# Kernel optimization log

Measured on AMD Instinct MI355X. Metric: run time of the kernel, lower is better.

Reference implementation:

```python
import jax, jax.numpy as jnp
import numpy as np

V = 25426          # tgt_vocab_size
D = 256            # d_model
H = 8              # heads
DH = 2048          # dim_head (d_ff passed positionally as d_head in source)
INNER = H * DH     # 16384
CLS = V            # cls token id (same value for t1 and t2 in source)
MASK_TOK = V + 2   # mask token id
VT = V + 3         # total embedding vocab


def _pos_encoding(n, d):
    pos = np.arange(n, dtype=np.float32)[:, None]
    div = np.exp(np.arange(0, d, 2, dtype=np.float32) * (-np.log(10000.0) / d))
    pe = np.zeros((n, d), dtype=np.float32)
    pe[:, 0::2] = np.sin(pos * div)
    pe[:, 1::2] = np.cos(pos * div)
    return jnp.asarray(pe)


def _layernorm(x, g, b, eps=1e-5):
    m = x.mean(-1, keepdims=True)
    v = ((x - m) ** 2).mean(-1, keepdims=True)
    return (x - m) / jnp.sqrt(v + eps) * g + b


def _cross_attn(x, ctx, pad_mask, Wq, Wk, Wv, Wo, bo):
    # x: [B,N,D], ctx: [B,M,Dc], pad_mask: [B,M] True = masked
    B, N, _ = x.shape
    M = ctx.shape[1]
    scale = DH ** -0.5
    q = (x @ Wq).reshape(B, N, H, DH)
    k = (ctx @ Wk).reshape(B, M, H, DH)
    v = (ctx @ Wv).reshape(B, M, H, DH)
    sim = jnp.einsum('bihd,bjhd->bhij', q, k) * scale  # [B,H,N,M]
    neg = -jnp.finfo(sim.dtype).max
    sim = jnp.where(pad_mask[:, None, None, :], neg, sim)
    attn = jax.nn.softmax(sim, axis=-1)
    out = jnp.einsum('bhij,bjhd->bihd', attn, v).reshape(B, N, INNER)
    return out @ Wo + bo


def _decoder(x, tgt_pad, src_mask, enc_output, p):
    a = _cross_attn(x, x, tgt_pad, p['Wq_s'], p['Wk_s'], p['Wv_s'], p['Wo_s'], p['bo_s'])
    x = _layernorm(x + a, p['g1'], p['be1'])
    a = _cross_attn(x, enc_output, src_mask, p['Wq_c'], p['Wk_c'], p['Wv_c'], p['Wo_c'], p['bo_c'])
    x = _layernorm(x + a, p['g2'], p['be2'])
    f = jax.nn.gelu(x @ p['W1'] + p['b1'], approximate=False) @ p['W2'] + p['b2']
    x = _layernorm(x + f, p['g3'], p['be3'])
    return x


def setup_inputs() -> dict:
    key = jax.random.key(0)
    ks = jax.random.split(key, 32)
    B, S, L = 2, 1024, 767
    d = {
        'src_input_id': jax.random.randint(ks[0], (B, S), 0, V),
        'tgt_input_id_t1': jax.random.randint(ks[1], (B, L), 0, V),
        'tgt_input_id_t2': jax.random.randint(ks[2], (B, L), 0, V),
        'original_lens': jax.random.randint(ks[3], (B,), 1, L),
        'enc_output': jax.random.normal(ks[4], (B, S, D), dtype=jnp.float32),
    }
    emb = jax.random.normal(ks[5], (VT, D), dtype=jnp.float32) * 0.02
    d['token_emb'] = emb.at[0].set(0.0)  # padding_idx=0
    s = 0.02
    d['Wq_s'] = jax.random.normal(ks[6], (D, INNER)) * s
    d['Wk_s'] = jax.random.normal(ks[7], (D, INNER)) * s
    d['Wv_s'] = jax.random.normal(ks[8], (D, INNER)) * s
    d['Wo_s'] = jax.random.normal(ks[9], (INNER, D)) * s
    d['bo_s'] = jnp.zeros((D,), jnp.float32)
    d['Wq_c'] = jax.random.normal(ks[10], (D, INNER)) * s
    d['Wk_c'] = jax.random.normal(ks[11], (D, INNER)) * s
    d['Wv_c'] = jax.random.normal(ks[12], (D, INNER)) * s
    d['Wo_c'] = jax.random.normal(ks[13], (INNER, D)) * s
    d['bo_c'] = jnp.zeros((D,), jnp.float32)
    d['W1'] = jax.random.normal(ks[14], (D, D)) * s  # Mlp hidden collapses to D (source bug)
    d['b1'] = jnp.zeros((D,), jnp.float32)
    d['W2'] = jax.random.normal(ks[15], (D, D)) * s
    d['b2'] = jnp.zeros((D,), jnp.float32)
    for i, n in enumerate(['g1', 'g2', 'g3']):
        d[n] = jnp.ones((D,), jnp.float32)
    for n in ['be1', 'be2', 'be3']:
        d[n] = jnp.zeros((D,), jnp.float32)
    d['Wfc'] = jax.random.normal(ks[16], (D, V)) * s
    d['bfc'] = jnp.zeros((V,), jnp.float32)
    return d


def reference(src_input_id, tgt_input_id_t1, tgt_input_id_t2, original_lens,
              enc_output, token_emb,
              Wq_s, Wk_s, Wv_s, Wo_s, bo_s,
              Wq_c, Wk_c, Wv_c, Wo_c, bo_c,
              W1, b1, W2, b2, g1, be1, g2, be2, g3, be3, Wfc, bfc):
    p = dict(Wq_s=Wq_s, Wk_s=Wk_s, Wv_s=Wv_s, Wo_s=Wo_s, bo_s=bo_s,
             Wq_c=Wq_c, Wk_c=Wk_c, Wv_c=Wv_c, Wo_c=Wo_c, bo_c=bo_c,
             W1=W1, b1=b1, W2=W2, b2=b2, g1=g1, be1=be1, g2=g2, be2=be2, g3=g3, be3=be3)
    B = tgt_input_id_t1.shape[0]
    cls = jnp.full((B, 1), CLS, dtype=tgt_input_id_t1.dtype)
    t1 = jnp.concatenate([cls, tgt_input_id_t1], axis=1)
    t2 = jnp.concatenate([cls, tgt_input_id_t2], axis=1)
    tgt = jnp.concatenate([t1, t2], axis=1)          # [B, T]
    tgt_pad = tgt == 0
    src_mask = src_input_id == 0
    # generate=True path: mask positions where id==mask_token or id==0
    tgt_mask = (tgt == MASK_TOK) | (tgt == 0)
    tgt_ids = jnp.where(tgt_mask, MASK_TOK, tgt)
    x = token_emb[tgt_ids]                            # [B, T, D]
    pe = _pos_encoding(x.shape[1], D)
    x = 2.0 * x + pe[None, :, :]                      # prepare_tokens: x + (x + pe), faithful to source
    x = _decoder(x, tgt_pad, src_mask, enc_output, p)
    logits = x @ Wfc + bfc
    return logits[:, 1:, :], x[:, 0, :]
```

## Files before the change

### kernel.cpp

```cpp
#include <hip/hip_runtime.h>
#include <hip/hip_bf16.h>
#include <float.h>
#include <math.h>

#define BB 2
#define SS 1024
#define LL 767
#define TT 1536
#define DD 256
#define HH 8
#define DHD 2048
#define INNER_ 16384
#define VV 25426
#define VPAD 25472
#define CLS_TOK 25426
#define MASK_TOKEN 25428
#define ROWS (BB*TT)
#define SROWS (BB*SS)

typedef __attribute__((ext_vector_type(8))) __bf16 bf16x8;
typedef __attribute__((ext_vector_type(4))) float f32x4;

__device__ __forceinline__ unsigned short f2bu(float f) {
    union { float f; unsigned u; } v; v.f = f;
    unsigned r = v.u + 0x7fff + ((v.u >> 16) & 1);
    return (unsigned short)(r >> 16);
}
__device__ __forceinline__ float bu2f(unsigned short u) {
    union { unsigned u; float f; } v; v.u = ((unsigned)u) << 16;
    return v.f;
}

__device__ __forceinline__ void gload16(const void* g, void* l) {
    __builtin_amdgcn_global_load_lds(
        (const __attribute__((address_space(1))) void*)g,
        (__attribute__((address_space(3))) void*)l, 16, 0, 0);
}


__global__ __launch_bounds__(256) void embed_kernel(
    const int* __restrict__ t1, const int* __restrict__ t2,
    const float* __restrict__ emb, float* __restrict__ x,
    unsigned short* __restrict__ xb, unsigned char* __restrict__ tgt_pad)
{
    int t = blockIdx.x, b = blockIdx.y, d = threadIdx.x;
    int raw;
    if (t == 0)            raw = CLS_TOK;
    else if (t <= LL)      raw = t1[b * LL + (t - 1)];
    else if (t == LL + 1)  raw = CLS_TOK;
    else                   raw = t2[b * LL + (t - LL - 2)];
    int id = (raw == 0 || raw == MASK_TOKEN) ? MASK_TOKEN : raw;
    int i = d >> 1;
    float ang = (float)t * expf(-0.03597789208f * (float)(2 * i));
    float pe = (d & 1) ? cosf(ang) : sinf(ang);
    float val = 2.f * emb[(long long)id * DD + d] + pe;
    long long idx = ((long long)(b * TT + t)) * DD + d;
    x[idx] = val;
    xb[idx] = f2bu(val);
    if (d == 0) tgt_pad[b * TT + t] = (raw == 0) ? 1 : 0;
}

__global__ __launch_bounds__(256) void masks_kernel(
    const int* __restrict__ src, unsigned char* __restrict__ m, int* __restrict__ rm)
{
    int i = blockIdx.x * 256 + threadIdx.x;
    if (i < SROWS) m[i] = (src[i] == 0) ? 1 : 0;
    if (i < ROWS) {
        int b = i / TT, t = i % TT;
        rm[i] = (t == 0) ? -1 : (b * (TT - 1) + t - 1);
    }
}

__global__ __launch_bounds__(256) void copycls_kernel(
    const float* __restrict__ x, float* __restrict__ out2)
{
    int b = blockIdx.x, d = threadIdx.x;
    out2[b * DD + d] = x[(long long)b * TT * DD + d];
}

__global__ __launch_bounds__(256) void conv_bf16v4(
    const float* __restrict__ in, unsigned short* __restrict__ out)
{
    size_t i = ((size_t)blockIdx.x * 256 + threadIdx.x) * 4;
    float4 v = *reinterpret_cast<const float4*>(in + i);
    ushort4 u;
    u.x = f2bu(v.x); u.y = f2bu(v.y); u.z = f2bu(v.z); u.w = f2bu(v.w);
    *reinterpret_cast<ushort4*>(out + i) = u;
}

__global__ __launch_bounds__(256) void convW6(
    const float* __restrict__ w0, const float* __restrict__ w1,
    const float* __restrict__ w2, const float* __restrict__ w3,
    const float* __restrict__ w4, const float* __restrict__ w5,
    unsigned short* __restrict__ dst)
{
    int seg = blockIdx.y;
    const float* s = seg == 0 ? w0 : seg == 1 ? w1 : seg == 2 ? w2 :
                     seg == 3 ? w3 : seg == 4 ? w4 : w5;
    size_t i = ((size_t)blockIdx.x * 256 + threadIdx.x) * 4;
    float4 v = *reinterpret_cast<const float4*>(s + i);
    ushort4 u;
    u.x = f2bu(v.x); u.y = f2bu(v.y); u.z = f2bu(v.z); u.w = f2bu(v.w);
    *reinterpret_cast<ushort4*>(dst + (size_t)seg * ((size_t)DD * INNER_) + i) = u;
}

__global__ __launch_bounds__(256) void transpose_conv(
    const float* __restrict__ in, unsigned short* __restrict__ out,
    int R, int Cin, int Nout)
{
    __shared__ float t[32][33];
    int k0 = blockIdx.x * 32, n0 = blockIdx.y * 32;
#pragma unroll
    for (int i = 0; i < 4; ++i) {
        int k = k0 + threadIdx.y + i * 8;
        int n = n0 + threadIdx.x;
        t[threadIdx.y + i * 8][threadIdx.x] = (n < Cin) ? in[(size_t)k * Cin + n] : 0.f;
    }
    __syncthreads();
#pragma unroll
    for (int i = 0; i < 4; ++i) {
        int n = n0 + threadIdx.y + i * 8;
        int k = k0 + threadIdx.x;
        out[(size_t)n * R + k] = f2bu(t[threadIdx.x][threadIdx.y + i * 8]);
    }
}

template<int STORE, int SPLITK>
__global__ __launch_bounds__(256) void gemm_bt(
    const unsigned short* __restrict__ A, int lda,
    const unsigned short* __restrict__ B, int ldb,
    void* __restrict__ Cv, int ldc,
    int M, int N, int K, float alpha, int zs,
    long long sAb, long long sAh, long long sBb, long long sBh,
    long long sCb, long long sCh,
    const float* __restrict__ bias, const int* __restrict__ rowmap)
{
    __shared__ unsigned short As[8192];
    __shared__ unsigned short Bs[8192];
    const int tid = threadIdx.x;
    const int w = tid >> 6, l = tid & 63;
    const int m0 = blockIdx.x * 128, n0 = blockIdx.y * 128;

    int kbeg = 0, kend = K;
    long long czoff = 0;
    if (SPLITK > 1) {
        constexpr int KSH = (SPLITK == 8) ? 3 : (SPLITK == 4) ? 2 : (SPLITK == 2) ? 1 : 0;
        int kidx = blockIdx.z & (SPLITK - 1);
        int zh = blockIdx.z >> KSH;
        int kc = K / SPLITK;
        kbeg = kidx * kc; kend = kbeg + kc;
        A += zh * sAh;
        B += zh * sBh;
        czoff = zh * sCh;
    } else {
        int zb = blockIdx.z >> zs;
        int zh = blockIdx.z - (zb << zs);
        A += zb * sAb + zh * sAh;
        B += zb * sBb + zh * sBh;
        czoff = zb * sCb + zh * sCh;
    }

    const int wr = (w >> 1) << 6, wc = (w & 1) << 6;
    const int lrow = l & 15, lk = l >> 4;

    const int sro = (w << 3) + (l >> 3);
    const int sko = (((l & 7) ^ (l >> 3)) << 3);
    const int ldst = (w << 10) + (l << 4);

    f32x4 acc[4][4];
#pragma unroll
    for (int mi = 0; mi < 4; ++mi)
#pragma unroll
        for (int ni = 0; ni < 4; ++ni)
            acc[mi][ni] = (f32x4){0.f, 0.f, 0.f, 0.f};

    for (int kt = kbeg; kt < kend; kt += 64) {
#pragma unroll
        for (int j = 0; j < 4; ++j)
            gload16(A + (size_t)(m0 + sro + j * 32) * lda + kt + sko,
                    (char*)As + (j << 12) + ldst);
#pragma unroll
        for (int j = 0; j < 4; ++j)
            gload16(B + (size_t)(n0 + sro + j * 32) * ldb + kt + sko,
                    (char*)Bs + (j << 12) + ldst);
        __syncthreads();

#pragma unroll
        for (int kk = 0; kk < 2; ++kk) {
            const int slot = (kk << 2) + lk;
            bf16x8 af[4], bfr[4];
#pragma unroll
            for (int mi = 0; mi < 4; ++mi) {
                int ra = wr + (mi << 4) + lrow;
                af[mi] = *reinterpret_cast<const bf16x8*>(
                    (const char*)As + (ra << 7) + ((slot ^ (ra & 7)) << 4));
            }
#pragma unroll
            for (int ni = 0; ni < 4; ++ni) {
                int rb = wc + (ni << 4) + lrow;
                bfr[ni] = *reinterpret_cast<const bf16x8*>(
                    (const char*)Bs + (rb << 7) + ((slot ^ (rb & 7)) << 4));
            }
#pragma unroll
            for (int mi = 0; mi < 4; ++mi)
#pragma unroll
                for (int ni = 0; ni < 4; ++ni)
                    acc[mi][ni] = __builtin_amdgcn_mfma_f32_16x16x32_bf16(
                        af[mi], bfr[ni], acc[mi][ni], 0, 0, 0);
        }
        __syncthreads();
    }

    if (STORE == 0) {
        unsigned short* C = (unsigned short*)Cv + czoff;
#pragma unroll
        for (int mi = 0; mi < 4; ++mi) {
            int r = m0 + wr + (mi << 4) + (lk << 2);
#pragma unroll
            for (int ni = 0; ni < 4; ++ni) {
                int c = n0 + wc + (ni << 4) + lrow;
#pragma unroll
                for (int q = 0; q < 4; ++q)
                    C[(size_t)(r + q) * ldc + c] = f2bu(acc[mi][ni][q] * alpha);
            }
        }
    } else if (STORE == 2) {
        float* C = (float*)Cv;
#pragma unroll
        for (int mi = 0; mi < 4; ++mi) {
            int r = m0 + wr + (mi << 4) + (lk << 2);
#pragma unroll
            for (int q = 0; q < 4; ++q) {
                int rm = rowmap[r + q];
                if (rm < 0) continue;
#pragma unroll
                for (int ni = 0; ni < 4; ++ni) {
                    int c = n0 + wc + (ni << 4) + lrow;
                    if (c < N) C[(size_t)rm * ldc + c] = acc[mi][ni][q] * alpha + bias[c];
                }
            }
        }
    } else {
        float* C = (float*)Cv + czoff;
#pragma unroll
        for (int mi = 0; mi < 4; ++mi) {
            int r = m0 + wr + (mi << 4) + (lk << 2);
#pragma unroll
            for (int ni = 0; ni < 4; ++ni) {
                int c = n0 + wc + (ni << 4) + lrow;
#pragma unroll
                for (int q = 0; q < 4; ++q)
                    atomicAdd(&C[(size_t)(r + q) * ldc + c], acc[mi][ni][q] * alpha);
            }
        }
    }
}

template<int CNT>
__global__ __launch_bounds__(256) void softmax_bf16(
    unsigned short* __restrict__ S, const unsigned char* __restrict__ mask, int zs)
{
    __shared__ float red[4];
    const int z = blockIdx.y;
    unsigned short* p = S + ((long long)z * TT + blockIdx.x) * (CNT * 256);
    const unsigned char* mk = mask + (long long)(z >> zs) * (CNT * 256);
    const int tid = threadIdx.x;

    float v[CNT];
    float mx = -FLT_MAX;
#pragma unroll
    for (int c = 0; c < CNT; ++c) {
        int j = (c << 8) + tid;
        float s = bu2f(p[j]);
        if (mk[j]) s = -FLT_MAX;
        v[c] = s;
        mx = fmaxf(mx, s);
    }
#pragma unroll
    for (int off = 32; off > 0; off >>= 1) mx = fmaxf(mx, __shfl_down(mx, off));
    if ((tid & 63) == 0) red[tid >> 6] = mx;
    __syncthreads();
    mx = fmaxf(fmaxf(red[0], red[1]), fmaxf(red[2], red[3]));
    __syncthreads();

    float sum = 0.f;
#pragma unroll
    for (int c = 0; c < CNT; ++c) {
        float e = expf(v[c] - mx);
        v[c] = e;
        sum += e;
    }
#pragma unroll
    for (int off = 32; off > 0; off >>= 1) sum += __shfl_down(sum, off);
    if ((tid & 63) == 0) red[tid >> 6] = sum;
    __syncthreads();
    sum = red[0] + red[1] + red[2] + red[3];
    float inv = 1.f / sum;
#pragma unroll
    for (int c = 0; c < CNT; ++c) p[(c << 8) + tid] = f2bu(v[c] * inv);
}

__global__ __launch_bounds__(256) void ln_kernel(
    float* __restrict__ x, const float* __restrict__ a,
    const float* __restrict__ abias,
    const float* __restrict__ g, const float* __restrict__ be,
    unsigned short* __restrict__ xb)
{
    __shared__ float red[4];
    const long long r = blockIdx.x;
    const int d = threadIdx.x;
    const long long idx = r * DD + d;
    float v = x[idx] + a[idx];
    if (abias) v += abias[d];

    float s = v;
#pragma unroll
    for (int off = 32; off > 0; off >>= 1) s += __shfl_down(s, off);
    if ((d & 63) == 0) red[d >> 6] = s;
    __syncthreads();
    float mean = (red[0] + red[1] + red[2] + red[3]) * (1.f / DD);
    __syncthreads();

    float df = v - mean;
    float s2 = df * df;
#pragma unroll
    for (int off = 32; off > 0; off >>= 1) s2 += __shfl_down(s2, off);
    if ((d & 63) == 0) red[d >> 6] = s2;
    __syncthreads();
    float var = (red[0] + red[1] + red[2] + red[3]) * (1.f / DD);

    float o = df / sqrtf(var + 1e-5f) * g[d] + be[d];
    x[idx] = o;
    xb[idx] = f2bu(o);
}

__global__ __launch_bounds__(256) void sgemm_small(
    const float* __restrict__ A, int lda,
    const float* __restrict__ Bm, int ldb,
    float* __restrict__ C, int ldc,
    int M, int N, int K, int mode, const float* __restrict__ bias)
{
    __shared__ float As[16][64];
    __shared__ float Bs[16][64];
    const int tid = threadIdx.x;
    const int tx = tid & 15, ty = tid >> 4;
    const int m0 = blockIdx.x * 64;
    const int n0 = blockIdx.y * 64;
    const int ar = tid >> 2, ak = (tid & 3) * 4;
    const int bk = tid >> 4, bn = (tid & 15) * 4;

    float acc[4][4];
#pragma unroll
    for (int i = 0; i < 4; ++i)
#pragma unroll
        for (int j = 0; j < 4; ++j) acc[i][j] = 0.f;

    for (int kt = 0; kt < K; kt += 16) {
        {
            const float4 va = *reinterpret_cast<const float4*>(
                A + (long long)(m0 + ar) * lda + (kt + ak));
            As[ak + 0][ar] = va.x; As[ak + 1][ar] = va.y;
            As[ak + 2][ar] = va.z; As[ak + 3][ar] = va.w;
        }
        {
            const float4 vb = *reinterpret_cast<const float4*>(
                Bm + (long long)(kt + bk) * ldb + (n0 + bn));
            *reinterpret_cast<float4*>(&Bs[bk][bn]) = vb;
        }
        __syncthreads();
#pragma unroll
        for (int k = 0; k < 16; ++k) {
            float a[4], b[4];
#pragma unroll
            for (int i = 0; i < 4; ++i) a[i] = As[k][ty + i * 16];
#pragma unroll
            for (int j = 0; j < 4; ++j) b[j] = Bs[k][tx + j * 16];
#pragma unroll
            for (int i = 0; i < 4; ++i)
#pragma unroll
                for (int j = 0; j < 4; ++j)
                    acc[i][j] = fmaf(a[i], b[j], acc[i][j]);
        }
        __syncthreads();
    }

#pragma unroll
    for (int i = 0; i < 4; ++i) {
        int r = m0 + ty + i * 16;
        float* crow = C + (long long)r * ldc;
#pragma unroll
        for (int j = 0; j < 4; ++j) {
            int n = n0 + tx + j * 16;
            float v = acc[i][j];
            if (mode >= 1) v += bias[n];
            if (mode == 2) v = 0.5f * v * (1.f + erff(v * 0.70710678118f));
            crow[n] = v;
        }
    }
}

extern "C" void kernel_launch(void* const* d_in, const int* in_sizes, int n_in,
                              void* d_out, int out_size, void* d_ws, size_t ws_size,
                              hipStream_t stream)
{
    const int*   src_ids = (const int*)d_in[0];
    const int*   t1      = (const int*)d_in[1];
    const int*   t2      = (const int*)d_in[2];
    const float* enc  = (const float*)d_in[4];
    const float* emb  = (const float*)d_in[5];
    const float* Wq_s = (const float*)d_in[6];
    const float* Wk_s = (const float*)d_in[7];
    const float* Wv_s = (const float*)d_in[8];
    const float* Wo_s = (const float*)d_in[9];
    const float* bo_s = (const float*)d_in[10];
    const float* Wq_c = (const float*)d_in[11];
    const float* Wk_c = (const float*)d_in[12];
    const float* Wv_c = (const float*)d_in[13];
    const float* Wo_c = (const float*)d_in[14];
    const float* bo_c = (const float*)d_in[15];
    const float* W1   = (const float*)d_in[16];
    const float* b1   = (const float*)d_in[17];
    const float* W2   = (const float*)d_in[18];
    const float* b2   = (const float*)d_in[19];
    const float* g1   = (const float*)d_in[20];
    const float* g2v  = (const float*)d_in[21];
    const float* g3   = (const float*)d_in[22];
    const float* be1  = (const float*)d_in[23];
    const float* be2  = (const float*)d_in[24];
    const float* be3  = (const float*)d_in[25];
    const float* Wfc  = (const float*)d_in[26];
    const float* bfc  = (const float*)d_in[27];

    char* p = (char*)d_ws;
    float* x    = (float*)p;           p += (size_t)ROWS * DD * 4;
    float* aout = (float*)p;           p += (size_t)ROWS * DD * 4;
    float* h1   = (float*)p;           p += (size_t)ROWS * DD * 4;
    unsigned short* xb   = (unsigned short*)p; p += (size_t)ROWS * DD * 2;
    unsigned short* xT   = (unsigned short*)p; p += (size_t)DD * ROWS * 2;
    unsigned short* encb = (unsigned short*)p; p += (size_t)SROWS * DD * 2;
    unsigned short* encT = (unsigned short*)p; p += (size_t)DD * SROWS * 2;
    unsigned short* Wqb_s = (unsigned short*)p; p += (size_t)DD * INNER_ * 2;
    unsigned short* Wkb_s = (unsigned short*)p; p += (size_t)DD * INNER_ * 2;
    unsigned short* Wvb_s = (unsigned short*)p; p += (size_t)DD * INNER_ * 2;
    unsigned short* Wqb_c = (unsigned short*)p; p += (size_t)DD * INNER_ * 2;
    unsigned short* Wkb_c = (unsigned short*)p; p += (size_t)DD * INNER_ * 2;
    unsigned short* Wvb_c = (unsigned short*)p; p += (size_t)DD * INNER_ * 2;
    unsigned short* WoTs  = (unsigned short*)p; p += (size_t)DD * INNER_ * 2;
    unsigned short* WoTc  = (unsigned short*)p; p += (size_t)DD * INNER_ * 2;
    unsigned short* WfcT  = (unsigned short*)p; p += (size_t)VPAD * DD * 2;
    unsigned short* MtNb  = (unsigned short*)p; p += (size_t)4 * 524288 * 2;
    unsigned char* tgtpad = (unsigned char*)p; p += ROWS;
    unsigned char* srcpad = (unsigned char*)p; p += SROWS;
    p = (char*)(((size_t)p + 15) & ~(size_t)15);
    int* rowmap = (int*)p;             p += (size_t)ROWS * 4;

    unsigned short* Mtb_s = MtNb;
    unsigned short* Ntb_s = MtNb + 524288;
    unsigned short* Mtb_c = MtNb + 2 * 524288;
    unsigned short* Ntb_c = MtNb + 3 * 524288;

    unsigned short* ob = (unsigned short*)d_out;
    unsigned short* simS = ob;
    unsigned short* Pb   = ob + 37748736;
    unsigned short* Ub   = Pb + 6291456;
    float* MNacc = (float*)d_out;

    embed_kernel<<<dim3(TT, BB), 256, 0, stream>>>(t1, t2, emb, x, xb, tgtpad);
    masks_kernel<<<dim3(ROWS / 256), 256, 0, stream>>>(src_ids, srcpad, rowmap);
    conv_bf16v4<<<dim3((SROWS * DD) / 1024), 256, 0, stream>>>(enc, encb);

    dim3 tcb(32, 8);
    transpose_conv<<<dim3(ROWS / 32, 8), tcb, 0, stream>>>(x, xT, ROWS, DD, DD);
    transpose_conv<<<dim3(SROWS / 32, 8), tcb, 0, stream>>>(enc, encT, SROWS, DD, DD);
    convW6<<<dim3((DD * INNER_) / 1024, 6), 256, 0, stream>>>(
        Wq_s, Wk_s, Wv_s, Wq_c, Wk_c, Wv_c, Wqb_s);
    transpose_conv<<<dim3(512, 8), tcb, 0, stream>>>(Wo_s, WoTs, INNER_, DD, DD);
    transpose_conv<<<dim3(512, 8), tcb, 0, stream>>>(Wo_c, WoTc, INNER_, DD, DD);
    transpose_conv<<<dim3(8, VPAD / 32), tcb, 0, stream>>>(Wfc, WfcT, DD, VV, VPAD);

    const float scale = 0.022097086912079608f;
    const long long Z0 = 0;

    hipMemsetAsync(MNacc, 0, (size_t)4 * 524288 * 4, stream);
    gemm_bt<3, 4><<<dim3(2, 2, 32), 256, 0, stream>>>(
        Wkb_s, INNER_, Wqb_s, INNER_, MNacc, 256, 256, 256, DHD, 1.f, 0,
        Z0, 2048, Z0, 2048, Z0, 65536, nullptr, nullptr);
    gemm_bt<3, 4><<<dim3(2, 2, 32), 256, 0, stream>>>(
        WoTs, INNER_, Wvb_s, INNER_, MNacc + 524288, 2048, 256, 256, DHD, 1.f, 0,
        Z0, 2048, Z0, 2048, Z0, 256, nullptr, nullptr);
    gemm_bt<3, 4><<<dim3(2, 2, 32), 256, 0, stream>>>(
        Wkb_c, INNER_, Wqb_c, INNER_, MNacc + 2 * 524288, 256, 256, 256, DHD, 1.f, 0,
        Z0, 2048, Z0, 2048, Z0, 65536, nullptr, nullptr);
    gemm_bt<3, 4><<<dim3(2, 2, 32), 256, 0, stream>>>(
        WoTc, INNER_, Wvb_c, INNER_, MNacc + 3 * 524288, 2048, 256, 256, DHD, 1.f, 0,
        Z0, 2048, Z0, 2048, Z0, 256, nullptr, nullptr);
    conv_bf16v4<<<dim3((4 * 524288) / 1024), 256, 0, stream>>>(MNacc, MtNb);

    hipMemsetAsync(aout, 0, (size_t)ROWS * DD * sizeof(float), stream);
    gemm_bt<0, 1><<<dim3(24, 2, 8), 256, 0, stream>>>(
        xb, DD, Mtb_s, DD, Pb, DD, ROWS, DD, DD, 1.f, 3,
        Z0, Z0, Z0, 65536, Z0, 786432, nullptr, nullptr);
    gemm_bt<0, 1><<<dim3(12, 12, 16), 256, 0, stream>>>(
        Pb, DD, xb, DD, simS, TT, TT, TT, DD, scale, 3,
        393216, 786432, 393216, Z0,
        18874368, 2359296, nullptr, nullptr);
    softmax_bf16<6><<<dim3(TT, 16), 256, 0, stream>>>(simS, tgtpad, 3);
    gemm_bt<0, 1><<<dim3(12, 2, 16), 256, 0, stream>>>(
        simS, TT, xT, ROWS, Ub, 2048, TT, DD, TT, 1.f, 3,
        18874368, 2359296, 1536, Z0,
        3145728, 256, nullptr, nullptr);
    gemm_bt<3, 4><<<dim3(24, 2, 4), 256, 0, stream>>>(
        Ub, 2048, Ntb_s, 2048, aout, DD, ROWS, DD, 2048, 1.f, 0,
        Z0, Z0, Z0, Z0, Z0, Z0, nullptr, nullptr);
    ln_kernel<<<dim3(ROWS), 256, 0, stream>>>(x, aout, bo_s, g1, be1, xb);

    hipMemsetAsync(aout, 0, (size_t)ROWS * DD * sizeof(float), stream);
    gemm_bt<0, 1><<<dim3(24, 2, 8), 256, 0, stream>>>(
        xb, DD, Mtb_c, DD, Pb, DD, ROWS, DD, DD, 1.f, 3,
        Z0, Z0, Z0, 65536, Z0, 786432, nullptr, nullptr);
    gemm_bt<0, 1><<<dim3(12, 8, 16), 256, 0, stream>>>(
        Pb, DD, encb, DD, simS, SS, TT, SS, DD, scale, 3,
        393216, 786432, 262144, Z0,
        12582912, 1572864, nullptr, nullptr);
    softmax_bf16<4><<<dim3(TT, 16), 256, 0, stream>>>(simS, srcpad, 3);
    gemm_bt<0, 1><<<dim3(12, 2, 16), 256, 0, stream>>>(
        simS, SS, encT, SROWS, Ub, 2048, TT, DD, SS, 1.f, 3,
        12582912, 1572864, 1024, Z0,
        3145728, 256, nullptr, nullptr);
    gemm_bt<3, 4><<<dim3(24, 2, 4), 256, 0, stream>>>(
        Ub, 2048, Ntb_c, 2048, aout, DD, ROWS, DD, 2048, 1.f, 0,
        Z0, Z0, Z0, Z0, Z0, Z0, nullptr, nullptr);
    ln_kernel<<<dim3(ROWS), 256, 0, stream>>>(x, aout, bo_c, g2v, be2, xb);

    sgemm_small<<<dim3(ROWS / 64, DD / 64, 1), 256, 0, stream>>>(
        x, DD, W1, DD, h1, DD, ROWS, DD, DD, 2, b1);
    sgemm_small<<<dim3(ROWS / 64, DD / 64, 1), 256, 0, stream>>>(
        h1, DD, W2, DD, aout, DD, ROWS, DD, DD, 0, nullptr);
    ln_kernel<<<dim3(ROWS), 256, 0, stream>>>(x, aout, b2, g3, be3, xb);

    gemm_bt<2, 1><<<dim3(24, VPAD / 128, 1), 256, 0, stream>>>(
        xb, DD, WfcT, DD, d_out, VV, ROWS, VV, DD, 1.f, 0,
        Z0, Z0, Z0, Z0, Z0, Z0, bfc, rowmap);

    copycls_kernel<<<dim3(BB), 256, 0, stream>>>(
        x, (float*)d_out + (long long)BB * (TT - 1) * VV);
}
```

Before: 639.1 us.

## Fold V·Wo projection before attention, use bf16 MFMA GEMMs for FFN

Reassociates the attention output path: instead of computing attn@V per head into a wide U buffer and then multiplying by Wo, it first projects context through the folded V·Wo matrix into a transposed per-head YT buffer, then the attn GEMM accumulates directly into the output via atomics. This removes the large U intermediate and the separate Wo GEMM, plus the x/enc transposes. The FFN fp32 sgemm is replaced by bf16 MFMA GEMMs with fused bias+GELU epilogue, and softmax is vectorized to two elements per thread. Risks include atomic contention across heads and reduced precision in the FFN.

New measurement: 634.4 us. Within noise of the previous version (-0.7%).

```diff
diff --git a/kernel.cpp b/kernel.cpp
--- a/kernel.cpp
+++ b/kernel.cpp
@@ -224,6 +224,22 @@
                     C[(size_t)(r + q) * ldc + c] = f2bu(acc[mi][ni][q] * alpha);
             }
         }
+    } else if (STORE == 1) {
+        unsigned short* C = (unsigned short*)Cv + czoff;
+#pragma unroll
+        for (int ni = 0; ni < 4; ++ni) {
+            int c = n0 + wc + (ni << 4) + lrow;
+#pragma unroll
+            for (int mi = 0; mi < 4; ++mi) {
+                int r = m0 + wr + (mi << 4) + (lk << 2);
+                ushort4 u;
+                u.x = f2bu(acc[mi][ni][0] * alpha);
+                u.y = f2bu(acc[mi][ni][1] * alpha);
+                u.z = f2bu(acc[mi][ni][2] * alpha);
+                u.w = f2bu(acc[mi][ni][3] * alpha);
+                *reinterpret_cast<ushort4*>(&C[(size_t)c * ldc + r]) = u;
+            }
+        }
     } else if (STORE == 2) {
         float* C = (float*)Cv;
 #pragma unroll
@@ -240,6 +256,35 @@
                 }
             }
         }
+    } else if (STORE == 3) {
+        float* C = (float*)Cv + czoff;
+#pragma unroll
+        for (int mi = 0; mi < 4; ++mi) {
+            int r = m0 + wr + (mi << 4) + (lk << 2);
+#pragma unroll
+            for (int ni = 0; ni < 4; ++ni) {
+                int c = n0 + wc + (ni << 4) + lrow;
+#pragma unroll
+                for (int q = 0; q < 4; ++q)
+                    atomicAdd(&C[(size_t)(r + q) * ldc + c], acc[mi][ni][q] * alpha);
+            }
+        }
+    } else if (STORE == 4) {
+        unsigned short* C = (unsigned short*)Cv + czoff;
+#pragma unroll
+        for (int mi = 0; mi < 4; ++mi) {
+            int r = m0 + wr + (mi << 4) + (lk << 2);
+#pragma unroll
+            for (int ni = 0; ni < 4; ++ni) {
+                int c = n0 + wc + (ni << 4) + lrow;
+#pragma unroll
+                for (int q = 0; q < 4; ++q) {
+                    float v = acc[mi][ni][q] * alpha + bias[c];
+                    v = 0.5f * v * (1.f + erff(v * 0.70710678118f));
+                    C[(size_t)(r + q) * ldc + c] = f2bu(v);
+                }
+            }
+        }
     } else {
         float* C = (float*)Cv + czoff;
 #pragma unroll
@@ -250,31 +295,34 @@
                 int c = n0 + wc + (ni << 4) + lrow;
 #pragma unroll
                 for (int q = 0; q < 4; ++q)
-                    atomicAdd(&C[(size_t)(r + q) * ldc + c], acc[mi][ni][q] * alpha);
-            }
-        }
-    }
-}
-
-template<int CNT>
+                    C[(size_t)(r + q) * ldc + c] = acc[mi][ni][q] * alpha;
+            }
+        }
+    }
+}
+
+template<int PPT>
 __global__ __launch_bounds__(256) void softmax_bf16(
     unsigned short* __restrict__ S, const unsigned char* __restrict__ mask, int zs)
 {
     __shared__ float red[4];
     const int z = blockIdx.y;
-    unsigned short* p = S + ((long long)z * TT + blockIdx.x) * (CNT * 256);
-    const unsigned char* mk = mask + (long long)(z >> zs) * (CNT * 256);
+    const int RL = PPT * 512;
+    ushort2* p = (ushort2*)(S + ((long long)z * TT + blockIdx.x) * RL);
+    const uchar2* mk = (const uchar2*)(mask + (long long)(z >> zs) * RL);
     const int tid = threadIdx.x;
 
-    float v[CNT];
+    float v[2 * PPT];
     float mx = -FLT_MAX;
 #pragma unroll
-    for (int c = 0; c < CNT; ++c) {
+    for (int c = 0; c < PPT; ++c) {
         int j = (c << 8) + tid;
-        float s = bu2f(p[j]);
-        if (mk[j]) s = -FLT_MAX;
-        v[c] = s;
-        mx = fmaxf(mx, s);
+        ushort2 u = p[j];
+        uchar2 mm = mk[j];
+        float s0 = mm.x ? -FLT_MAX : bu2f(u.x);
+        float s1 = mm.y ? -FLT_MAX : bu2f(u.y);
+        v[2 * c] = s0; v[2 * c + 1] = s1;
+        mx = fmaxf(mx, fmaxf(s0, s1));
     }
 #pragma unroll
     for (int off = 32; off > 0; off >>= 1) mx = fmaxf(mx, __shfl_down(mx, off));
@@ -285,7 +333,7 @@
 
     float sum = 0.f;
 #pragma unroll
-    for (int c = 0; c < CNT; ++c) {
+    for (int c = 0; c < 2 * PPT; ++c) {
         float e = expf(v[c] - mx);
         v[c] = e;
         sum += e;
@@ -297,7 +345,13 @@
     sum = red[0] + red[1] + red[2] + red[3];
     float inv = 1.f / sum;
 #pragma unroll
-    for (int c = 0; c < CNT; ++c) p[(c << 8) + tid] = f2bu(v[c] * inv);
+    for (int c = 0; c < PPT; ++c) {
+        int j = (c << 8) + tid;
+        ushort2 u;
+        u.x = f2bu(v[2 * c] * inv);
+        u.y = f2bu(v[2 * c + 1] * inv);
+        p[j] = u;
+    }
 }
 
 __global__ __launch_bounds__(256) void ln_kernel(
@@ -332,71 +386,6 @@
     float o = df / sqrtf(var + 1e-5f) * g[d] + be[d];
     x[idx] = o;
     xb[idx] = f2bu(o);
-}
-
-__global__ __launch_bounds__(256) void sgemm_small(
-    const float* __restrict__ A, int lda,
-    const float* __restrict__ Bm, int ldb,
-    float* __restrict__ C, int ldc,
-    int M, int N, int K, int mode, const float* __restrict__ bias)
-{
-    __shared__ float As[16][64];
-    __shared__ float Bs[16][64];
-    const int tid = threadIdx.x;
-    const int tx = tid & 15, ty = tid >> 4;
-    const int m0 = blockIdx.x * 64;
-    const int n0 = blockIdx.y * 64;
-    const int ar = tid >> 2, ak = (tid & 3) * 4;
-    const int bk = tid >> 4, bn = (tid & 15) * 4;
-
-    float acc[4][4];
-#pragma unroll
-    for (int i = 0; i < 4; ++i)
-#pragma unroll
-        for (int j = 0; j < 4; ++j) acc[i][j] = 0.f;
-
-    for (int kt = 0; kt < K; kt += 16) {
-        {
-            const float4 va = *reinterpret_cast<const float4*>(
-                A + (long long)(m0 + ar) * lda + (kt + ak));
-            As[ak + 0][ar] = va.x; As[ak + 1][ar] = va.y;
-            As[ak + 2][ar] = va.z; As[ak + 3][ar] = va.w;
-        }
-        {
-            const float4 vb = *reinterpret_cast<const float4*>(
-                Bm + (long long)(kt + bk) * ldb + (n0 + bn));
-            *reinterpret_cast<float4*>(&Bs[bk][bn]) = vb;
-        }
-        __syncthreads();
-#pragma unroll
-        for (int k = 0; k < 16; ++k) {
-            float a[4], b[4];
-#pragma unroll
-            for (int i = 0; i < 4; ++i) a[i] = As[k][ty + i * 16];
-#pragma unroll
-            for (int j = 0; j < 4; ++j) b[j] = Bs[k][tx + j * 16];
-#pragma unroll
-            for (int i = 0; i < 4; ++i)
-#pragma unroll
-                for (int j = 0; j < 4; ++j)
-                    acc[i][j] = fmaf(a[i], b[j], acc[i][j]);
-        }
-        __syncthreads();
-    }
-
-#pragma unroll
-    for (int i = 0; i < 4; ++i) {
-        int r = m0 + ty + i * 16;
-        float* crow = C + (long long)r * ldc;
-#pragma unroll
-        for (int j = 0; j < 4; ++j) {
-            int n = n0 + tx + j * 16;
-            float v = acc[i][j];
-            if (mode >= 1) v += bias[n];
-            if (mode == 2) v = 0.5f * v * (1.f + erff(v * 0.70710678118f));
-            crow[n] = v;
-        }
-    }
 }
 
 extern "C" void kernel_launch(void* const* d_in, const int* in_sizes, int n_in,
@@ -434,11 +423,9 @@
     char* p = (char*)d_ws;
     float* x    = (float*)p;           p += (size_t)ROWS * DD * 4;
     float* aout = (float*)p;           p += (size_t)ROWS * DD * 4;
-    float* h1   = (float*)p;           p += (size_t)ROWS * DD * 4;
+    unsigned short* h1b  = (unsigned short*)p; p += (size_t)ROWS * DD * 2;
     unsigned short* xb   = (unsigned short*)p; p += (size_t)ROWS * DD * 2;
-    unsigned short* xT   = (unsigned short*)p; p += (size_t)DD * ROWS * 2;
     unsigned short* encb = (unsigned short*)p; p += (size_t)SROWS * DD * 2;
-    unsigned short* encT = (unsigned short*)p; p += (size_t)DD * SROWS * 2;
     unsigned short* Wqb_s = (unsigned short*)p; p += (size_t)DD * INNER_ * 2;
     unsigned short* Wkb_s = (unsigned short*)p; p += (size_t)DD * INNER_ * 2;
     unsigned short* Wvb_s = (unsigned short*)p; p += (size_t)DD * INNER_ * 2;
@@ -448,6 +435,8 @@
     unsigned short* WoTs  = (unsigned short*)p; p += (size_t)DD * INNER_ * 2;
     unsigned short* WoTc  = (unsigned short*)p; p += (size_t)DD * INNER_ * 2;
     unsigned short* WfcT  = (unsigned short*)p; p += (size_t)VPAD * DD * 2;
+    unsigned short* W1Tb  = (unsigned short*)p; p += (size_t)DD * DD * 2;
+    unsigned short* W2Tb  = (unsigned short*)p; p += (size_t)DD * DD * 2;
     unsigned short* MtNb  = (unsigned short*)p; p += (size_t)4 * 524288 * 2;
     unsigned char* tgtpad = (unsigned char*)p; p += ROWS;
     unsigned char* srcpad = (unsigned char*)p; p += SROWS;
@@ -462,7 +451,7 @@
     unsigned short* ob = (unsigned short*)d_out;
     unsigned short* simS = ob;
     unsigned short* Pb   = ob + 37748736;
-    unsigned short* Ub   = Pb + 6291456;
+    unsigned short* YTb  = Pb + 6291456;
     float* MNacc = (float*)d_out;
 
     embed_kernel<<<dim3(TT, BB), 256, 0, stream>>>(t1, t2, emb, x, xb, tgtpad);
@@ -470,13 +459,13 @@
     conv_bf16v4<<<dim3((SROWS * DD) / 1024), 256, 0, stream>>>(enc, encb);
 
     dim3 tcb(32, 8);
-    transpose_conv<<<dim3(ROWS / 32, 8), tcb, 0, stream>>>(x, xT, ROWS, DD, DD);
-    transpose_conv<<<dim3(SROWS / 32, 8), tcb, 0, stream>>>(enc, encT, SROWS, DD, DD);
     convW6<<<dim3((DD * INNER_) / 1024, 6), 256, 0, stream>>>(
         Wq_s, Wk_s, Wv_s, Wq_c, Wk_c, Wv_c, Wqb_s);
     transpose_conv<<<dim3(512, 8), tcb, 0, stream>>>(Wo_s, WoTs, INNER_, DD, DD);
     transpose_conv<<<dim3(512, 8), tcb, 0, stream>>>(Wo_c, WoTc, INNER_, DD, DD);
     transpose_conv<<<dim3(8, VPAD / 32), tcb, 0, stream>>>(Wfc, WfcT, DD, VV, VPAD);
+    transpose_conv<<<dim3(8, 8), tcb, 0, stream>>>(W1, W1Tb, DD, DD, DD);
+    transpose_conv<<<dim3(8, 8), tcb, 0, stream>>>(W2, W2Tb, DD, DD, DD);
 
     const float scale = 0.022097086912079608f;
     const long long Z0 = 0;
@@ -500,42 +489,44 @@
     gemm_bt<0, 1><<<dim3(24, 2, 8), 256, 0, stream>>>(
         xb, DD, Mtb_s, DD, Pb, DD, ROWS, DD, DD, 1.f, 3,
         Z0, Z0, Z0, 65536, Z0, 786432, nullptr, nullptr);
+    gemm_bt<1, 1><<<dim3(24, 2, 8), 256, 0, stream>>>(
+        xb, DD, Ntb_s, 2048, YTb, ROWS, ROWS, DD, DD, 1.f, 3,
+        Z0, Z0, Z0, 256, Z0, 786432, nullptr, nullptr);
     gemm_bt<0, 1><<<dim3(12, 12, 16), 256, 0, stream>>>(
         Pb, DD, xb, DD, simS, TT, TT, TT, DD, scale, 3,
         393216, 786432, 393216, Z0,
         18874368, 2359296, nullptr, nullptr);
-    softmax_bf16<6><<<dim3(TT, 16), 256, 0, stream>>>(simS, tgtpad, 3);
-    gemm_bt<0, 1><<<dim3(12, 2, 16), 256, 0, stream>>>(
-        simS, TT, xT, ROWS, Ub, 2048, TT, DD, TT, 1.f, 3,
-        18874368, 2359296, 1536, Z0,
-        3145728, 256, nullptr, nullptr);
-    gemm_bt<3, 4><<<dim3(24, 2, 4), 256, 0, stream>>>(
-        Ub, 2048, Ntb_s, 2048, aout, DD, ROWS, DD, 2048, 1.f, 0,
-        Z0, Z0, Z0, Z0, Z0, Z0, nullptr, nullptr);
+    softmax_bf16<3><<<dim3(TT, 16), 256, 0, stream>>>(simS, tgtpad, 3);
+    gemm_bt<3, 1><<<dim3(12, 2, 16), 256, 0, stream>>>(
+        simS, TT, YTb, ROWS, aout, DD, TT, DD, TT, 1.f, 3,
+        18874368, 2359296, 1536, 786432,
+        393216, Z0, nullptr, nullptr);
     ln_kernel<<<dim3(ROWS), 256, 0, stream>>>(x, aout, bo_s, g1, be1, xb);
 
     hipMemsetAsync(aout, 0, (size_t)ROWS * DD * sizeof(float), stream);
     gemm_bt<0, 1><<<dim3(24, 2, 8), 256, 0, stream>>>(
         xb, DD, Mtb_c, DD, Pb, DD, ROWS, DD, DD, 1.f, 3,
         Z0, Z0, Z0, 65536, Z0, 786432, nullptr, nullptr);
+    gemm_bt<1, 1><<<dim3(16, 2, 8), 256, 0, stream>>>(
+        encb, DD, Ntb_c, 2048, YTb, SROWS, SROWS, DD, DD, 1.f, 3,
+        Z0, Z0, Z0, 256, Z0, 524288, nullptr, nullptr);
     gemm_bt<0, 1><<<dim3(12, 8, 16), 256, 0, stream>>>(
         Pb, DD, encb, DD, simS, SS, TT, SS, DD, scale, 3,
         393216, 786432, 262144, Z0,
         12582912, 1572864, nullptr, nullptr);
-    softmax_bf16<4><<<dim3(TT, 16), 256, 0, stream>>>(simS, srcpad, 3);
-    gemm_bt<0, 1><<<dim3(12, 2, 16), 256, 0, stream>>>(
-        simS, SS, encT, SROWS, Ub, 2048, TT, DD, SS, 1.f, 3,
-        12582912, 1572864, 1024, Z0,
-        3145728, 256, nullptr, nullptr);
-    gemm_bt<3, 4><<<dim3(24, 2, 4), 256, 0, stream>>>(
-        Ub, 2048, Ntb_c, 2048, aout, DD, ROWS, DD, 2048, 1.f, 0,
+    softmax_bf16<2><<<dim3(TT, 16), 256, 0, stream>>>(simS, srcpad, 3);
+    gemm_bt<3, 1><<<dim3(12, 2, 16), 256, 0, stream>>>(
+        simS, SS, YTb, SROWS, aout, DD, TT, DD, SS, 1.f, 3,
+        12582912, 1572864, 1024, 524288,
+        393216, Z0, nullptr, nullptr);
+    ln_kernel<<<dim3(ROWS), 256, 0, stream>>>(x, aout, bo_c, g2v, be2, xb);
+
+    gemm_bt<4, 1><<<dim3(24, 2, 1), 256, 0, stream>>>(
+        xb, DD, W1Tb, DD, h1b, DD, ROWS, DD, DD, 1.f, 0,
+        Z0, Z0, Z0, Z0, Z0, Z0, b1, nullptr);
+    gemm_bt<5, 1><<<dim3(24, 2, 1), 256, 0, stream>>>(
+        h1b, DD, W2Tb, DD, aout, DD, ROWS, DD, DD, 1.f, 0,
         Z0, Z0, Z0, Z0, Z0, Z0, nullptr, nullptr);
-    ln_kernel<<<dim3(ROWS), 256, 0, stream>>>(x, aout, bo_c, g2v, be2, xb);
-
-    sgemm_small<<<dim3(ROWS / 64, DD / 64, 1), 256, 0, stream>>>(
-        x, DD, W1, DD, h1, DD, ROWS, DD, DD, 2, b1);
-    sgemm_small<<<dim3(ROWS / 64, DD / 64, 1), 256, 0, stream>>>(
-        h1, DD, W2, DD, aout, DD, ROWS, DD, DD, 0, nullptr);
     ln_kernel<<<dim3(ROWS), 256, 0, stream>>>(x, aout, b2, g3, be3, xb);
 
     gemm_bt<2, 1><<<dim3(24, VPAD / 128, 1), 256, 0, stream>>>(
```
